# Optimization experiments

Hardware: AMD Instinct MI355X
Metric: run time of the kernel (lower is better)

Reference implementation:

```python
import jax, jax.numpy as jnp
import numpy as np

N, K = 1024, 128


def setup_inputs() -> dict:
    key = jax.random.key(0)
    k0, k1, k2, k3, k4 = jax.random.split(key, 5)
    beta = jax.random.uniform(k0, (N, N), dtype=jnp.float32)  # attention weights
    # omega must be invertible: small perturbation of identity, well-conditioned
    omega = jax.random.normal(k1, (N, K, K), dtype=jnp.float32) * 0.1 + jnp.eye(K, dtype=jnp.float32)
    # precisions are SPD in the physical model: A A^T / K + I
    A = jax.random.normal(k2, (N, K, K), dtype=jnp.float32)
    precision_p = jnp.einsum('nij,nkj->nik', A, A) / K + jnp.eye(K, dtype=jnp.float32)
    B = jax.random.normal(k3, (N, K, K), dtype=jnp.float32)
    precision_q = jnp.einsum('nij,nkj->nik', B, B) / K + jnp.eye(K, dtype=jnp.float32)
    C = jax.random.normal(k4, (K, K), dtype=jnp.float32)
    obs_precision = C @ C.T / K + jnp.eye(K, dtype=jnp.float32)
    return {
        'beta': beta,
        'omega': omega,
        'precision_p': precision_p,
        'precision_q': precision_q,
        'obs_precision': obs_precision,
    }


def reference(beta, omega, precision_p, precision_q, obs_precision):
    """Vectorized effective_mass_diagonal (Eq. 37).

    M_i = Lp_i + sum_{k!=i} beta_ik * Om_ik^{-T} Lq_k Om_ik^{-1}
               + (sum_{j!=i} beta_ji) * Lq_i + obs_precision
    with Om_ik = Om_i Om_k^{-1}, so Om_ik^{-1} = Om_k Om_i^{-1} and the
    sandwiched term factors as Om_i^{-T} (sum_k beta_ik * Om_k^T Lq_k Om_k) Om_i^{-1},
    turning the O(N^2) tiny-inverse loop into batched GEMMs + N inverses.
    """
    n = beta.shape[0]
    eye_mask = 1.0 - jnp.eye(n, dtype=beta.dtype)
    beta_nd = beta * eye_mask  # zero diagonal (k==i and j==i skipped)

    omega_inv = jnp.linalg.inv(omega)  # (N,K,K), batched
    # S_k = Omega_k^T Lq_k Omega_k, shape (N,K,K)
    S = jnp.einsum('nji,njk,nkl->nil', omega, precision_q, omega)
    # weighted accumulation over k != i: (N,N) x (N,K,K) -> (N,K,K)
    W = jnp.einsum('ik,kab->iab', beta_nd, S)
    # sandwich with Omega_i^{-T} ... Omega_i^{-1}
    cross = jnp.einsum('nji,njk,nkl->nil', omega_inv, W, omega_inv)

    col_sum = beta_nd.sum(axis=0)  # sum_j beta_ji, shape (N,)
    M = precision_p + cross + col_sum[:, None, None] * precision_q + obs_precision[None, :, :]
    return M  # (N, K, K)
```

## Files before the change

kernel.cpp:

```cpp
#include <hip/hip_runtime.h>

#define NN 1024
#define KK 128

typedef __attribute__((ext_vector_type(8))) short bf16x8;
typedef __attribute__((ext_vector_type(4))) float f32x4;
typedef __attribute__((ext_vector_type(8))) unsigned short u16x8;

__device__ __forceinline__ unsigned int bf16rne(float x) {
    unsigned int u = __float_as_uint(x);
    return (u + 0x7FFFu + ((u >> 16) & 1u)) >> 16;
}

__device__ __forceinline__ void split8(const float* xs, bf16x8& h8, bf16x8& l8) {
    #pragma unroll
    for (int j = 0; j < 8; ++j) {
        unsigned int hb = bf16rne(xs[j]);
        float hf = __uint_as_float(hb << 16);
        h8[j] = (short)hb;
        l8[j] = (short)bf16rne(xs[j] - hf);
    }
}

template<bool FINAL>
__global__ __launch_bounds__(512) void sandwich_mfma(
    const float* __restrict__ A_, const float* __restrict__ B_,
    float* __restrict__ Out,
    const float* __restrict__ Lp, const float* __restrict__ Lq,
    const float* __restrict__ obs, const float* __restrict__ beta)
{
    __shared__ short lds_buf[69632];
    short* Bth = lds_buf;
    short* Btl = lds_buf + 17408;
    short* Tth = lds_buf + 34816;
    short* Ttl = lds_buf + 52224;
    float* pan = (float*)(lds_buf + 34816);
    float* rowblk_  = (float*)(lds_buf + 34816);
    float* rowstar_ = rowblk_ + 1056;
    float* cpan_    = rowstar_ + 1056;
    __shared__ float wred[8];
    __shared__ float cs_sh;

    const int n    = blockIdx.x;
    const int tid  = threadIdx.x;
    const int lane = tid & 63;
    const int wid  = tid >> 6;
    const int wr   = wid >> 1;
    const int wc   = wid & 1;
    const int lm   = lane & 15;
    const int lk   = lane >> 4;
    const size_t base = (size_t)n * (KK * KK);

    if (FINAL) {
        float s = 0.f;
        for (int j = tid; j < NN; j += 512)
            if (j != n) s += beta[(size_t)j * NN + n];
        #pragma unroll
        for (int off = 32; off >= 1; off >>= 1) s += __shfl_down(s, off);
        if (lane == 0) wred[wid] = s;
        __syncthreads();
        if (tid == 0) {
            float t = 0.f;
            #pragma unroll
            for (int w = 0; w < 8; ++w) t += wred[w];
            cs_sh = t;
        }
    }

    if constexpr (!FINAL) {
        #pragma unroll
        for (int cp = 0; cp < 2; ++cp) {
            #pragma unroll
            for (int it = 0; it < 4; ++it) {
                int gid = it * 512 + tid;
                int k   = gid >> 4;
                int c4  = (gid & 15) * 4;
                *(float4*)&pan[k * 66 + c4] =
                    *(const float4*)(B_ + base + (size_t)k * KK + cp * 64 + c4);
            }
            __syncthreads();
            #pragma unroll
            for (int it = 0; it < 2; ++it) {
                int t  = it * 512 + tid;
                int c  = t >> 4;
                int ko = (t & 15) * 8;
                float xs[8];
                #pragma unroll
                for (int j = 0; j < 8; ++j) xs[j] = pan[(ko + j) * 66 + c];
                bf16x8 h8, l8;
                split8(xs, h8, l8);
                const int gc = cp * 64 + c;
                *(bf16x8*)&Bth[gc * 136 + ko] = h8;
                *(bf16x8*)&Btl[gc * 136 + ko] = l8;
            }
            __syncthreads();
        }
    } else {
        const int rg = tid >> 4;
        const int cg = tid & 15;
        const int r0 = rg * 4;
        const int c0 = cg * 8;

        float4 a4[4][2];
        #pragma unroll
        for (int i = 0; i < 4; ++i) {
            const float* src = B_ + base + (size_t)(r0 + i) * KK + c0;
            a4[i][0] = *(const float4*)(src);
            a4[i][1] = *(const float4*)(src + 4);
        }

        for (int g = 0; g < 32; ++g) {
            const int buf = g & 1;
            const int pgc = g >> 1;
            const int sub = g & 1;
            float* RB = rowblk_ + buf * 528;
            float* RS = rowstar_ + buf * 528;
            float* CP = cpan_ + buf * 512;

            if (rg == g) {
                #pragma unroll
                for (int p = 0; p < 4; ++p) {
                    *(float4*)&RB[p * 132 + c0]     = a4[p][0];
                    *(float4*)&RB[p * 132 + c0 + 4] = a4[p][1];
                }
            }
            if (cg == pgc) {
                if (sub == 0) {
                    #pragma unroll
                    for (int i = 0; i < 4; ++i)
                        *(float4*)&CP[(r0 + i) * 4] = a4[i][0];
                } else {
                    #pragma unroll
                    for (int i = 0; i < 4; ++i)
                        *(float4*)&CP[(r0 + i) * 4] = a4[i][1];
                }
            }
            __syncthreads();

            float4 p0 = *(const float4*)&RB[0 * 132 + 4 * g];
            float4 p1 = *(const float4*)&RB[1 * 132 + 4 * g];
            float4 p2 = *(const float4*)&RB[2 * 132 + 4 * g];
            float4 p3 = *(const float4*)&RB[3 * 132 + 4 * g];
            const float s0 = p0.x*p1.y - p1.x*p0.y;
            const float s1 = p0.x*p1.z - p1.x*p0.z;
            const float s2 = p0.x*p1.w - p1.x*p0.w;
            const float s3 = p0.y*p1.z - p1.y*p0.z;
            const float s4 = p0.y*p1.w - p1.y*p0.w;
            const float s5 = p0.z*p1.w - p1.z*p0.w;
            const float c5 = p2.z*p3.w - p3.z*p2.w;
            const float c4 = p2.y*p3.w - p3.y*p2.w;
            const float c3 = p2.y*p3.z - p3.y*p2.z;
            const float c2 = p2.x*p3.w - p3.x*p2.w;
            const float c1 = p2.x*p3.z - p3.x*p2.z;
            const float c0f = p2.x*p3.y - p3.x*p2.y;
            const float det = s0*c5 - s1*c4 + s2*c3 + s3*c2 - s4*c1 + s5*c0f;
            const float id  = 1.0f / det;

            {
                const int c = tid & 127;
                const float r0v = RB[0 * 132 + c];
                const float r1v = RB[1 * 132 + c];
                const float r2v = RB[2 * 132 + c];
                const float r3v = RB[3 * 132 + c];
                const int cl = c - 4 * g;
                const int pq = tid >> 7;
                if (pq == 0) {
                    const float Pi0 = ( p1.y*c5 - p1.z*c4 + p1.w*c3) * id;
                    const float Pi1 = (-p0.y*c5 + p0.z*c4 - p0.w*c3) * id;
                    const float Pi2 = ( p3.y*s5 - p3.z*s4 + p3.w*s3) * id;
                    const float Pi3 = (-p2.y*s5 + p2.z*s4 - p2.w*s3) * id;
                    float v = Pi0*r0v + Pi1*r1v + Pi2*r2v + Pi3*r3v;
                    if      (cl == 0) v += Pi0;
                    else if (cl == 1) v += Pi1;
                    else if (cl == 2) v += Pi2;
                    else if (cl == 3) v += Pi3;
                    RS[0 * 132 + c] = v;
                } else if (pq == 1) {
                    const float Pi0 = (-p1.x*c5 + p1.z*c2 - p1.w*c1) * id;
                    const float Pi1 = ( p0.x*c5 - p0.z*c2 + p0.w*c1) * id;
                    const float Pi2 = (-p3.x*s5 + p3.z*s2 - p3.w*s1) * id;
                    const float Pi3 = ( p2.x*s5 - p2.z*s2 + p2.w*s1) * id;
                    float v = Pi0*r0v + Pi1*r1v + Pi2*r2v + Pi3*r3v;
                    if      (cl == 0) v += Pi0;
                    else if (cl == 1) v += Pi1;
                    else if (cl == 2) v += Pi2;
                    else if (cl == 3) v += Pi3;
                    RS[1 * 132 + c] = v;
                } else if (pq == 2) {
                    const float Pi0 = ( p1.x*c4 - p1.y*c2 + p1.w*c0f) * id;
                    const float Pi1 = (-p0.x*c4 + p0.y*c2 - p0.w*c0f) * id;
                    const float Pi2 = ( p3.x*s4 - p3.y*s2 + p3.w*s0) * id;
                    const float Pi3 = (-p2.x*s4 + p2.y*s2 - p2.w*s0) * id;
                    float v = Pi0*r0v + Pi1*r1v + Pi2*r2v + Pi3*r3v;
                    if      (cl == 0) v += Pi0;
                    else if (cl == 1) v += Pi1;
                    else if (cl == 2) v += Pi2;
                    else if (cl == 3) v += Pi3;
                    RS[2 * 132 + c] = v;
                } else {
                    const float Pi0 = (-p1.x*c3 + p1.y*c1 - p1.z*c0f) * id;
                    const float Pi1 = ( p0.x*c3 - p0.y*c1 + p0.z*c0f) * id;
                    const float Pi2 = (-p3.x*s3 + p3.y*s1 - p3.z*s0) * id;
                    const float Pi3 = ( p2.x*s3 - p2.y*s1 + p2.z*s0) * id;
                    float v = Pi0*r0v + Pi1*r1v + Pi2*r2v + Pi3*r3v;
                    if      (cl == 0) v += Pi0;
                    else if (cl == 1) v += Pi1;
                    else if (cl == 2) v += Pi2;
                    else if (cl == 3) v += Pi3;
                    RS[3 * 132 + c] = v;
                }
            }
            __syncthreads();

            const bool piv_rg = (rg == g);
            #pragma unroll
            for (int h = 0; h < 2; ++h) {
                const int ch = c0 + h * 4;
                float4 rs0 = *(const float4*)&RS[0 * 132 + ch];
                float4 rs1 = *(const float4*)&RS[1 * 132 + ch];
                float4 rs2 = *(const float4*)&RS[2 * 132 + ch];
                float4 rs3 = *(const float4*)&RS[3 * 132 + ch];
                #pragma unroll
                for (int i = 0; i < 4; ++i) {
                    float4 f = *(const float4*)&CP[(r0 + i) * 4];
                    if (piv_rg) {
                        if (i == 0) f.x -= 1.0f;
                        else if (i == 1) f.y -= 1.0f;
                        else if (i == 2) f.z -= 1.0f;
                        else f.w -= 1.0f;
                    }
                    a4[i][h].x = fmaf(-f.x, rs0.x, fmaf(-f.y, rs1.x, fmaf(-f.z, rs2.x, fmaf(-f.w, rs3.x, a4[i][h].x))));
                    a4[i][h].y = fmaf(-f.x, rs0.y, fmaf(-f.y, rs1.y, fmaf(-f.z, rs2.y, fmaf(-f.w, rs3.y, a4[i][h].y))));
                    a4[i][h].z = fmaf(-f.x, rs0.z, fmaf(-f.y, rs1.z, fmaf(-f.z, rs2.z, fmaf(-f.w, rs3.z, a4[i][h].z))));
                    a4[i][h].w = fmaf(-f.x, rs0.w, fmaf(-f.y, rs1.w, fmaf(-f.z, rs2.w, fmaf(-f.w, rs3.w, a4[i][h].w))));
                }
            }
        }
        __syncthreads();

        #pragma unroll
        for (int i = 0; i < 4; ++i) {
            const int row = r0 + i;
            #pragma unroll
            for (int h = 0; h < 2; ++h) {
                float xs[4] = {a4[i][h].x, a4[i][h].y, a4[i][h].z, a4[i][h].w};
                #pragma unroll
                for (int j = 0; j < 4; ++j) {
                    const int col = c0 + h * 4 + j;
                    unsigned int hb = bf16rne(xs[j]);
                    Bth[col * 136 + row] = (short)hb;
                    Btl[col * 136 + row] =
                        (short)bf16rne(xs[j] - __uint_as_float(hb << 16));
                }
            }
        }
        __syncthreads();
    }

    f32x4 acc[2][4];
    #pragma unroll
    for (int a = 0; a < 2; ++a)
        #pragma unroll
        for (int b = 0; b < 4; ++b) acc[a][b] = (f32x4){0.f, 0.f, 0.f, 0.f};

    #pragma unroll 1
    for (int ks = 0; ks < 4; ++ks) {
        const int k0 = ks * 32;
        bf16x8 afh[2], afl[2], bfh[4], bfl[4];
        #pragma unroll
        for (int rt = 0; rt < 2; ++rt) {
            const int r = wr * 32 + rt * 16 + lm;
            const float* ap = A_ + base + (size_t)r * KK + k0 + lk * 8;
            float4 x0 = *(const float4*)ap;
            float4 x1 = *(const float4*)(ap + 4);
            float xs[8] = {x0.x, x0.y, x0.z, x0.w, x1.x, x1.y, x1.z, x1.w};
            split8(xs, afh[rt], afl[rt]);
        }
        #pragma unroll
        for (int ct = 0; ct < 4; ++ct) {
            const int c = wc * 64 + ct * 16 + lm;
            bfh[ct] = *(const bf16x8*)&Bth[c * 136 + k0 + lk * 8];
            bfl[ct] = *(const bf16x8*)&Btl[c * 136 + k0 + lk * 8];
        }
        #pragma unroll
        for (int rt = 0; rt < 2; ++rt)
            #pragma unroll
            for (int ct = 0; ct < 4; ++ct) {
                acc[rt][ct] = __builtin_amdgcn_mfma_f32_16x16x32_bf16(
                    afh[rt], bfh[ct], acc[rt][ct], 0, 0, 0);
                acc[rt][ct] = __builtin_amdgcn_mfma_f32_16x16x32_bf16(
                    afh[rt], bfl[ct], acc[rt][ct], 0, 0, 0);
                acc[rt][ct] = __builtin_amdgcn_mfma_f32_16x16x32_bf16(
                    afl[rt], bfh[ct], acc[rt][ct], 0, 0, 0);
            }
    }

    #pragma unroll
    for (int rt = 0; rt < 2; ++rt)
        #pragma unroll
        for (int ct = 0; ct < 4; ++ct) {
            const int col  = wc * 64 + ct * 16 + lm;
            const int row0 = wr * 32 + rt * 16 + lk * 4;
            unsigned short h[4], l[4];
            #pragma unroll
            for (int j = 0; j < 4; ++j) {
                float x = acc[rt][ct][j];
                unsigned int hb = bf16rne(x);
                h[j] = (unsigned short)hb;
                l[j] = (unsigned short)bf16rne(x - __uint_as_float(hb << 16));
            }
            *(ushort4*)&Tth[col * 136 + row0] = make_ushort4(h[0], h[1], h[2], h[3]);
            *(ushort4*)&Ttl[col * 136 + row0] = make_ushort4(l[0], l[1], l[2], l[3]);
        }
    __syncthreads();

    f32x4 acc2[2][4];
    #pragma unroll
    for (int a = 0; a < 2; ++a)
        #pragma unroll
        for (int b = 0; b < 4; ++b) acc2[a][b] = (f32x4){0.f, 0.f, 0.f, 0.f};

    #pragma unroll 1
    for (int ks = 0; ks < 4; ++ks) {
        const int k0 = ks * 32;
        bf16x8 afh[2], afl[2], bfh[4], bfl[4];
        #pragma unroll
        for (int rt = 0; rt < 2; ++rt) {
            const int r = wr * 32 + rt * 16 + lm;
            afh[rt] = *(const bf16x8*)&Bth[r * 136 + k0 + lk * 8];
            afl[rt] = *(const bf16x8*)&Btl[r * 136 + k0 + lk * 8];
        }
        #pragma unroll
        for (int ct = 0; ct < 4; ++ct) {
            const int c = wc * 64 + ct * 16 + lm;
            bfh[ct] = *(const bf16x8*)&Tth[c * 136 + k0 + lk * 8];
            bfl[ct] = *(const bf16x8*)&Ttl[c * 136 + k0 + lk * 8];
        }
        #pragma unroll
        for (int rt = 0; rt < 2; ++rt)
            #pragma unroll
            for (int ct = 0; ct < 4; ++ct) {
                acc2[rt][ct] = __builtin_amdgcn_mfma_f32_16x16x32_bf16(
                    afh[rt], bfh[ct], acc2[rt][ct], 0, 0, 0);
                acc2[rt][ct] = __builtin_amdgcn_mfma_f32_16x16x32_bf16(
                    afh[rt], bfl[ct], acc2[rt][ct], 0, 0, 0);
                acc2[rt][ct] = __builtin_amdgcn_mfma_f32_16x16x32_bf16(
                    afl[rt], bfh[ct], acc2[rt][ct], 0, 0, 0);
            }
    }

    const float csv = FINAL ? cs_sh : 0.f;
    #pragma unroll
    for (int rt = 0; rt < 2; ++rt)
        #pragma unroll
        for (int ct = 0; ct < 4; ++ct) {
            const int col  = wc * 64 + ct * 16 + lm;
            const int row0 = wr * 32 + rt * 16 + lk * 4;
            #pragma unroll
            for (int j = 0; j < 4; ++j) {
                const int row = row0 + j;
                float o = acc2[rt][ct][j];
                if (FINAL) {
                    o += Lp[base + (size_t)row * KK + col]
                       + csv * Lq[base + (size_t)row * KK + col]
                       + obs[(size_t)row * KK + col];
                }
                Out[base + (size_t)row * KK + col] = o;
            }
        }
}

__global__ __launch_bounds__(256) void split_transpose_kernel(
    const float* __restrict__ S,
    unsigned short* __restrict__ Th, unsigned short* __restrict__ Tl)
{
    __shared__ float tile[128][132];
    const int tid = threadIdx.x;
    const int c0  = blockIdx.x * 128;
    const int k0  = blockIdx.y * 128;

    #pragma unroll
    for (int it = 0; it < 16; ++it) {
        int gid = it * 256 + tid;
        int kk  = gid >> 5;
        int c4  = (gid & 31) * 4;
        float4 v = *(const float4*)(S + (size_t)(k0 + kk) * 16384 + c0 + c4);
        *(float4*)&tile[kk][c4] = v;
    }
    __syncthreads();
    #pragma unroll
    for (int it = 0; it < 8; ++it) {
        int gid = it * 256 + tid;
        int c   = gid >> 4;
        int kc  = (gid & 15) * 8;
        u16x8 h, l;
        #pragma unroll
        for (int j = 0; j < 8; ++j) {
            float x = tile[kc + j][c];
            unsigned int hb = bf16rne(x);
            float hf = __uint_as_float(hb << 16);
            h[j] = (unsigned short)hb;
            l[j] = (unsigned short)bf16rne(x - hf);
        }
        size_t o = (size_t)(c0 + c) * 1024 + k0 + kc;
        *(u16x8*)(Th + o) = h;
        *(u16x8*)(Tl + o) = l;
    }
}

__global__ __launch_bounds__(256) void beta_split_kernel(
    const float* __restrict__ beta,
    unsigned short* __restrict__ Bh, unsigned short* __restrict__ Bl)
{
    const int gid = blockIdx.x * 256 + threadIdx.x;
    const int r   = gid >> 8;
    const int c4  = (gid & 255) * 4;
    float4 v = *(const float4*)(beta + (size_t)r * NN + c4);
    if (r == c4 + 0) v.x = 0.f;
    if (r == c4 + 1) v.y = 0.f;
    if (r == c4 + 2) v.z = 0.f;
    if (r == c4 + 3) v.w = 0.f;
    float xs[4] = {v.x, v.y, v.z, v.w};
    unsigned short hs[4], ls[4];
    #pragma unroll
    for (int j = 0; j < 4; ++j) {
        unsigned int hb = bf16rne(xs[j]);
        hs[j] = (unsigned short)hb;
        ls[j] = (unsigned short)bf16rne(xs[j] - __uint_as_float(hb << 16));
    }
    *(ushort4*)(Bh + (size_t)r * NN + c4) = make_ushort4(hs[0], hs[1], hs[2], hs[3]);
    *(ushort4*)(Bl + (size_t)r * NN + c4) = make_ushort4(ls[0], ls[1], ls[2], ls[3]);
}

template<bool PRESPLIT>
__global__ __launch_bounds__(256) void gemm_beta_mfma(
    const float* __restrict__ beta,
    const unsigned short* __restrict__ Bth_g,
    const unsigned short* __restrict__ Btl_g,
    const unsigned short* __restrict__ Sth,
    const unsigned short* __restrict__ Stl,
    float* __restrict__ W)
{
    __shared__ unsigned short Ah[128][44], Al[128][44];
    __shared__ unsigned short Bh[128][44], Bl[128][44];

    const int tid  = threadIdx.x;
    const int lane = tid & 63;
    const int wid  = tid >> 6;
    const int wr   = wid >> 1, wc = wid & 1;
    const int lm   = lane & 15;
    const int lk   = lane >> 4;
    const int i0   = blockIdx.y * 128;
    const int cb   = blockIdx.x * 128;

    f32x4 acc[4][4];
    #pragma unroll
    for (int a = 0; a < 4; ++a)
        #pragma unroll
        for (int b = 0; b < 4; ++b) acc[a][b] = (f32x4){0.f, 0.f, 0.f, 0.f};

    for (int k0 = 0; k0 < 1024; k0 += 32) {
        if (PRESPLIT) {
            #pragma unroll
            for (int it = 0; it < 2; ++it) {
                int gid = it * 256 + tid;
                int r   = gid >> 2;
                int kc  = (gid & 3) * 8;
                size_t o = (size_t)(i0 + r) * NN + k0 + kc;
                *(u16x8*)&Ah[r][kc] = *(const u16x8*)(Bth_g + o);
                *(u16x8*)&Al[r][kc] = *(const u16x8*)(Btl_g + o);
            }
        } else {
            #pragma unroll
            for (int it = 0; it < 4; ++it) {
                int gid = it * 256 + tid;
                int r   = gid >> 3;
                int c4  = (gid & 7) * 4;
                int gi  = i0 + r;
                float4 v = *(const float4*)(beta + (size_t)gi * NN + k0 + c4);
                if (gi == k0 + c4 + 0) v.x = 0.f;
                if (gi == k0 + c4 + 1) v.y = 0.f;
                if (gi == k0 + c4 + 2) v.z = 0.f;
                if (gi == k0 + c4 + 3) v.w = 0.f;
                float xs[4] = {v.x, v.y, v.z, v.w};
                unsigned short hs[4], ls[4];
                #pragma unroll
                for (int j = 0; j < 4; ++j) {
                    unsigned int hb = bf16rne(xs[j]);
                    hs[j] = (unsigned short)hb;
                    ls[j] = (unsigned short)bf16rne(xs[j] - __uint_as_float(hb << 16));
                }
                *(ushort4*)&Ah[r][c4] = make_ushort4(hs[0], hs[1], hs[2], hs[3]);
                *(ushort4*)&Al[r][c4] = make_ushort4(ls[0], ls[1], ls[2], ls[3]);
            }
        }
        #pragma unroll
        for (int it = 0; it < 2; ++it) {
            int gid = it * 256 + tid;
            int c   = gid >> 2;
            int kc  = (gid & 3) * 8;
            size_t o = (size_t)(cb + c) * 1024 + k0 + kc;
            *(u16x8*)&Bh[c][kc] = *(const u16x8*)(Sth + o);
            *(u16x8*)&Bl[c][kc] = *(const u16x8*)(Stl + o);
        }
        __syncthreads();

        bf16x8 afh[4], afl[4], bfh[4], bfl[4];
        #pragma unroll
        for (int rt = 0; rt < 4; ++rt) {
            const int r = wr * 64 + rt * 16 + lm;
            afh[rt] = *(const bf16x8*)&Ah[r][lk * 8];
            afl[rt] = *(const bf16x8*)&Al[r][lk * 8];
        }
        #pragma unroll
        for (int ct = 0; ct < 4; ++ct) {
            const int c = wc * 64 + ct * 16 + lm;
            bfh[ct] = *(const bf16x8*)&Bh[c][lk * 8];
            bfl[ct] = *(const bf16x8*)&Bl[c][lk * 8];
        }
        #pragma unroll
        for (int rt = 0; rt < 4; ++rt)
            #pragma unroll
            for (int ct = 0; ct < 4; ++ct) {
                acc[rt][ct] = __builtin_amdgcn_mfma_f32_16x16x32_bf16(
                    afh[rt], bfh[ct], acc[rt][ct], 0, 0, 0);
                acc[rt][ct] = __builtin_amdgcn_mfma_f32_16x16x32_bf16(
                    afh[rt], bfl[ct], acc[rt][ct], 0, 0, 0);
                acc[rt][ct] = __builtin_amdgcn_mfma_f32_16x16x32_bf16(
                    afl[rt], bfh[ct], acc[rt][ct], 0, 0, 0);
            }
        __syncthreads();
    }

    #pragma unroll
    for (int rt = 0; rt < 4; ++rt)
        #pragma unroll
        for (int ct = 0; ct < 4; ++ct) {
            const int col = cb + wc * 64 + ct * 16 + lm;
            #pragma unroll
            for (int j = 0; j < 4; ++j) {
                const int row = i0 + wr * 64 + rt * 16 + lk * 4 + j;
                W[(size_t)row * 16384 + col] = acc[rt][ct][j];
            }
        }
}

extern "C" void kernel_launch(void* const* d_in, const int* in_sizes, int n_in,
                              void* d_out, int out_size, void* d_ws, size_t ws_size,
                              hipStream_t stream)
{
    const float* beta  = (const float*)d_in[0];
    const float* omega = (const float*)d_in[1];
    const float* Lp    = (const float*)d_in[2];
    const float* Lq    = (const float*)d_in[3];
    const float* obs   = (const float*)d_in[4];
    float* out = (float*)d_out;

    const size_t MATE = (size_t)NN * KK * KK;

    if (ws_size >= 2 * MATE * sizeof(float)) {
        float* S = (float*)d_ws;
        unsigned short* Sth = (unsigned short*)((char*)d_ws + MATE * sizeof(float));
        unsigned short* Stl = Sth + MATE;
        unsigned short* Bh  = (unsigned short*)d_ws;
        unsigned short* Bl  = Bh + (size_t)NN * NN;
        float* Wbuf = out;

        sandwich_mfma<false><<<dim3(NN), dim3(512), 0, stream>>>(
            Lq, omega, S, nullptr, nullptr, nullptr, nullptr);
        split_transpose_kernel<<<dim3(128, 8), dim3(256), 0, stream>>>(S, Sth, Stl);
        beta_split_kernel<<<dim3(1024), dim3(256), 0, stream>>>(beta, Bh, Bl);
        gemm_beta_mfma<true><<<dim3(128, 8), dim3(256), 0, stream>>>(
            beta, Bh, Bl, Sth, Stl, Wbuf);
        sandwich_mfma<true><<<dim3(NN), dim3(512), 0, stream>>>(
            Wbuf, omega, out, Lp, Lq, obs, beta);
    } else {
        float* S = (float*)d_ws;
        unsigned short* Sth = (unsigned short*)out;
        unsigned short* Stl = Sth + MATE;
        float* Wbuf = (float*)d_ws;

        sandwich_mfma<false><<<dim3(NN), dim3(512), 0, stream>>>(
            Lq, omega, S, nullptr, nullptr, nullptr, nullptr);
        split_transpose_kernel<<<dim3(128, 8), dim3(256), 0, stream>>>(S, Sth, Stl);
        gemm_beta_mfma<false><<<dim3(128, 8), dim3(256), 0, stream>>>(
            beta, nullptr, nullptr, Sth, Stl, Wbuf);
        sandwich_mfma<true><<<dim3(NN), dim3(512), 0, stream>>>(
            Wbuf, omega, out, Lp, Lq, obs, beta);
    }
}
```

Before: 451.2 us.

## Move omega inversion out of final sandwich and co-schedule it with beta GEMM

```diff
diff --git a/kernel.cpp b/kernel.cpp
--- a/kernel.cpp
+++ b/kernel.cpp
@@ -35,9 +35,6 @@
     short* Tth = lds_buf + 34816;
     short* Ttl = lds_buf + 52224;
     float* pan = (float*)(lds_buf + 34816);
-    float* rowblk_  = (float*)(lds_buf + 34816);
-    float* rowstar_ = rowblk_ + 1056;
-    float* cpan_    = rowstar_ + 1056;
     __shared__ float wred[8];
     __shared__ float cs_sh;
 
@@ -67,192 +64,30 @@
         }
     }
 
-    if constexpr (!FINAL) {
-        #pragma unroll
-        for (int cp = 0; cp < 2; ++cp) {
-            #pragma unroll
-            for (int it = 0; it < 4; ++it) {
-                int gid = it * 512 + tid;
-                int k   = gid >> 4;
-                int c4  = (gid & 15) * 4;
-                *(float4*)&pan[k * 66 + c4] =
-                    *(const float4*)(B_ + base + (size_t)k * KK + cp * 64 + c4);
-            }
-            __syncthreads();
-            #pragma unroll
-            for (int it = 0; it < 2; ++it) {
-                int t  = it * 512 + tid;
-                int c  = t >> 4;
-                int ko = (t & 15) * 8;
-                float xs[8];
-                #pragma unroll
-                for (int j = 0; j < 8; ++j) xs[j] = pan[(ko + j) * 66 + c];
-                bf16x8 h8, l8;
-                split8(xs, h8, l8);
-                const int gc = cp * 64 + c;
-                *(bf16x8*)&Bth[gc * 136 + ko] = h8;
-                *(bf16x8*)&Btl[gc * 136 + ko] = l8;
-            }
-            __syncthreads();
-        }
-    } else {
-        const int rg = tid >> 4;
-        const int cg = tid & 15;
-        const int r0 = rg * 4;
-        const int c0 = cg * 8;
-
-        float4 a4[4][2];
-        #pragma unroll
-        for (int i = 0; i < 4; ++i) {
-            const float* src = B_ + base + (size_t)(r0 + i) * KK + c0;
-            a4[i][0] = *(const float4*)(src);
-            a4[i][1] = *(const float4*)(src + 4);
-        }
-
-        for (int g = 0; g < 32; ++g) {
-            const int buf = g & 1;
-            const int pgc = g >> 1;
-            const int sub = g & 1;
-            float* RB = rowblk_ + buf * 528;
-            float* RS = rowstar_ + buf * 528;
-            float* CP = cpan_ + buf * 512;
-
-            if (rg == g) {
-                #pragma unroll
-                for (int p = 0; p < 4; ++p) {
-                    *(float4*)&RB[p * 132 + c0]     = a4[p][0];
-                    *(float4*)&RB[p * 132 + c0 + 4] = a4[p][1];
-                }
-            }
-            if (cg == pgc) {
-                if (sub == 0) {
-                    #pragma unroll
-                    for (int i = 0; i < 4; ++i)
-                        *(float4*)&CP[(r0 + i) * 4] = a4[i][0];
-                } else {
-                    #pragma unroll
-                    for (int i = 0; i < 4; ++i)
-                        *(float4*)&CP[(r0 + i) * 4] = a4[i][1];
-                }
-            }
-            __syncthreads();
-
-            float4 p0 = *(const float4*)&RB[0 * 132 + 4 * g];
-            float4 p1 = *(const float4*)&RB[1 * 132 + 4 * g];
-            float4 p2 = *(const float4*)&RB[2 * 132 + 4 * g];
-            float4 p3 = *(const float4*)&RB[3 * 132 + 4 * g];
-            const float s0 = p0.x*p1.y - p1.x*p0.y;
-            const float s1 = p0.x*p1.z - p1.x*p0.z;
-            const float s2 = p0.x*p1.w - p1.x*p0.w;
-            const float s3 = p0.y*p1.z - p1.y*p0.z;
-            const float s4 = p0.y*p1.w - p1.y*p0.w;
-            const float s5 = p0.z*p1.w - p1.z*p0.w;
-            const float c5 = p2.z*p3.w - p3.z*p2.w;
-            const float c4 = p2.y*p3.w - p3.y*p2.w;
-            const float c3 = p2.y*p3.z - p3.y*p2.z;
-            const float c2 = p2.x*p3.w - p3.x*p2.w;
-            const float c1 = p2.x*p3.z - p3.x*p2.z;
-            const float c0f = p2.x*p3.y - p3.x*p2.y;
-            const float det = s0*c5 - s1*c4 + s2*c3 + s3*c2 - s4*c1 + s5*c0f;
-            const float id  = 1.0f / det;
-
-            {
-                const int c = tid & 127;
-                const float r0v = RB[0 * 132 + c];
-                const float r1v = RB[1 * 132 + c];
-                const float r2v = RB[2 * 132 + c];
-                const float r3v = RB[3 * 132 + c];
-                const int cl = c - 4 * g;
-                const int pq = tid >> 7;
-                if (pq == 0) {
-                    const float Pi0 = ( p1.y*c5 - p1.z*c4 + p1.w*c3) * id;
-                    const float Pi1 = (-p0.y*c5 + p0.z*c4 - p0.w*c3) * id;
-                    const float Pi2 = ( p3.y*s5 - p3.z*s4 + p3.w*s3) * id;
-                    const float Pi3 = (-p2.y*s5 + p2.z*s4 - p2.w*s3) * id;
-                    float v = Pi0*r0v + Pi1*r1v + Pi2*r2v + Pi3*r3v;
-                    if      (cl == 0) v += Pi0;
-                    else if (cl == 1) v += Pi1;
-                    else if (cl == 2) v += Pi2;
-                    else if (cl == 3) v += Pi3;
-                    RS[0 * 132 + c] = v;
-                } else if (pq == 1) {
-                    const float Pi0 = (-p1.x*c5 + p1.z*c2 - p1.w*c1) * id;
-                    const float Pi1 = ( p0.x*c5 - p0.z*c2 + p0.w*c1) * id;
-                    const float Pi2 = (-p3.x*s5 + p3.z*s2 - p3.w*s1) * id;
-                    const float Pi3 = ( p2.x*s5 - p2.z*s2 + p2.w*s1) * id;
-                    float v = Pi0*r0v + Pi1*r1v + Pi2*r2v + Pi3*r3v;
-                    if      (cl == 0) v += Pi0;
-                    else if (cl == 1) v += Pi1;
-                    else if (cl == 2) v += Pi2;
-                    else if (cl == 3) v += Pi3;
-                    RS[1 * 132 + c] = v;
-                } else if (pq == 2) {
-                    const float Pi0 = ( p1.x*c4 - p1.y*c2 + p1.w*c0f) * id;
-                    const float Pi1 = (-p0.x*c4 + p0.y*c2 - p0.w*c0f) * id;
-                    const float Pi2 = ( p3.x*s4 - p3.y*s2 + p3.w*s0) * id;
-                    const float Pi3 = (-p2.x*s4 + p2.y*s2 - p2.w*s0) * id;
-                    float v = Pi0*r0v + Pi1*r1v + Pi2*r2v + Pi3*r3v;
-                    if      (cl == 0) v += Pi0;
-                    else if (cl == 1) v += Pi1;
-                    else if (cl == 2) v += Pi2;
-                    else if (cl == 3) v += Pi3;
-                    RS[2 * 132 + c] = v;
-                } else {
-                    const float Pi0 = (-p1.x*c3 + p1.y*c1 - p1.z*c0f) * id;
-                    const float Pi1 = ( p0.x*c3 - p0.y*c1 + p0.z*c0f) * id;
-                    const float Pi2 = (-p3.x*s3 + p3.y*s1 - p3.z*s0) * id;
-                    const float Pi3 = ( p2.x*s3 - p2.y*s1 + p2.z*s0) * id;
-                    float v = Pi0*r0v + Pi1*r1v + Pi2*r2v + Pi3*r3v;
-                    if      (cl == 0) v += Pi0;
-                    else if (cl == 1) v += Pi1;
-                    else if (cl == 2) v += Pi2;
-                    else if (cl == 3) v += Pi3;
-                    RS[3 * 132 + c] = v;
-                }
-            }
-            __syncthreads();
-
-            const bool piv_rg = (rg == g);
-            #pragma unroll
-            for (int h = 0; h < 2; ++h) {
-                const int ch = c0 + h * 4;
-                float4 rs0 = *(const float4*)&RS[0 * 132 + ch];
-                float4 rs1 = *(const float4*)&RS[1 * 132 + ch];
-                float4 rs2 = *(const float4*)&RS[2 * 132 + ch];
-                float4 rs3 = *(const float4*)&RS[3 * 132 + ch];
-                #pragma unroll
-                for (int i = 0; i < 4; ++i) {
-                    float4 f = *(const float4*)&CP[(r0 + i) * 4];
-                    if (piv_rg) {
-                        if (i == 0) f.x -= 1.0f;
-                        else if (i == 1) f.y -= 1.0f;
-                        else if (i == 2) f.z -= 1.0f;
-                        else f.w -= 1.0f;
-                    }
-                    a4[i][h].x = fmaf(-f.x, rs0.x, fmaf(-f.y, rs1.x, fmaf(-f.z, rs2.x, fmaf(-f.w, rs3.x, a4[i][h].x))));
-                    a4[i][h].y = fmaf(-f.x, rs0.y, fmaf(-f.y, rs1.y, fmaf(-f.z, rs2.y, fmaf(-f.w, rs3.y, a4[i][h].y))));
-                    a4[i][h].z = fmaf(-f.x, rs0.z, fmaf(-f.y, rs1.z, fmaf(-f.z, rs2.z, fmaf(-f.w, rs3.z, a4[i][h].z))));
-                    a4[i][h].w = fmaf(-f.x, rs0.w, fmaf(-f.y, rs1.w, fmaf(-f.z, rs2.w, fmaf(-f.w, rs3.w, a4[i][h].w))));
-                }
-            }
-        }
-        __syncthreads();
-
-        #pragma unroll
-        for (int i = 0; i < 4; ++i) {
-            const int row = r0 + i;
-            #pragma unroll
-            for (int h = 0; h < 2; ++h) {
-                float xs[4] = {a4[i][h].x, a4[i][h].y, a4[i][h].z, a4[i][h].w};
-                #pragma unroll
-                for (int j = 0; j < 4; ++j) {
-                    const int col = c0 + h * 4 + j;
-                    unsigned int hb = bf16rne(xs[j]);
-                    Bth[col * 136 + row] = (short)hb;
-                    Btl[col * 136 + row] =
-                        (short)bf16rne(xs[j] - __uint_as_float(hb << 16));
-                }
-            }
+    #pragma unroll
+    for (int cp = 0; cp < 2; ++cp) {
+        #pragma unroll
+        for (int it = 0; it < 4; ++it) {
+            int gid = it * 512 + tid;
+            int k   = gid >> 4;
+            int c4  = (gid & 15) * 4;
+            *(float4*)&pan[k * 66 + c4] =
+                *(const float4*)(B_ + base + (size_t)k * KK + cp * 64 + c4);
+        }
+        __syncthreads();
+        #pragma unroll
+        for (int it = 0; it < 2; ++it) {
+            int t  = it * 512 + tid;
+            int c  = t >> 4;
+            int ko = (t & 15) * 8;
+            float xs[8];
+            #pragma unroll
+            for (int j = 0; j < 8; ++j) xs[j] = pan[(ko + j) * 66 + c];
+            bf16x8 h8, l8;
+            split8(xs, h8, l8);
+            const int gc = cp * 64 + c;
+            *(bf16x8*)&Bth[gc * 136 + ko] = h8;
+            *(bf16x8*)&Btl[gc * 136 + ko] = l8;
         }
         __syncthreads();
     }
@@ -408,118 +243,73 @@
     }
 }
 
-__global__ __launch_bounds__(256) void beta_split_kernel(
+__device__ __forceinline__ void gemm_body(
     const float* __restrict__ beta,
-    unsigned short* __restrict__ Bh, unsigned short* __restrict__ Bl)
-{
-    const int gid = blockIdx.x * 256 + threadIdx.x;
-    const int r   = gid >> 8;
-    const int c4  = (gid & 255) * 4;
-    float4 v = *(const float4*)(beta + (size_t)r * NN + c4);
-    if (r == c4 + 0) v.x = 0.f;
-    if (r == c4 + 1) v.y = 0.f;
-    if (r == c4 + 2) v.z = 0.f;
-    if (r == c4 + 3) v.w = 0.f;
-    float xs[4] = {v.x, v.y, v.z, v.w};
-    unsigned short hs[4], ls[4];
-    #pragma unroll
-    for (int j = 0; j < 4; ++j) {
-        unsigned int hb = bf16rne(xs[j]);
-        hs[j] = (unsigned short)hb;
-        ls[j] = (unsigned short)bf16rne(xs[j] - __uint_as_float(hb << 16));
-    }
-    *(ushort4*)(Bh + (size_t)r * NN + c4) = make_ushort4(hs[0], hs[1], hs[2], hs[3]);
-    *(ushort4*)(Bl + (size_t)r * NN + c4) = make_ushort4(ls[0], ls[1], ls[2], ls[3]);
-}
-
-template<bool PRESPLIT>
-__global__ __launch_bounds__(256) void gemm_beta_mfma(
-    const float* __restrict__ beta,
-    const unsigned short* __restrict__ Bth_g,
-    const unsigned short* __restrict__ Btl_g,
     const unsigned short* __restrict__ Sth,
     const unsigned short* __restrict__ Stl,
-    float* __restrict__ W)
-{
-    __shared__ unsigned short Ah[128][44], Al[128][44];
-    __shared__ unsigned short Bh[128][44], Bl[128][44];
-
-    const int tid  = threadIdx.x;
+    float* __restrict__ W,
+    int cb_blk, int ib_blk, int tid, char* smem)
+{
+    unsigned short* Ah = (unsigned short*)smem;
+    unsigned short* Al = Ah + 128 * 44;
+    unsigned short* Bh = Al + 128 * 44;
+    unsigned short* Bl = Bh + 128 * 44;
+
     const int lane = tid & 63;
     const int wid  = tid >> 6;
-    const int wr   = wid >> 1, wc = wid & 1;
+    const int wr   = wid >> 1;
+    const int wc   = wid & 1;
     const int lm   = lane & 15;
     const int lk   = lane >> 4;
-    const int i0   = blockIdx.y * 128;
-    const int cb   = blockIdx.x * 128;
-
-    f32x4 acc[4][4];
-    #pragma unroll
-    for (int a = 0; a < 4; ++a)
+    const int i0   = ib_blk * 128;
+    const int cbase = cb_blk * 128;
+
+    f32x4 acc[2][4];
+    #pragma unroll
+    for (int a = 0; a < 2; ++a)
         #pragma unroll
         for (int b = 0; b < 4; ++b) acc[a][b] = (f32x4){0.f, 0.f, 0.f, 0.f};
 
+    const int ar = tid >> 2;
+    const int akc = (tid & 3) * 8;
+
     for (int k0 = 0; k0 < 1024; k0 += 32) {
-        if (PRESPLIT) {
-            #pragma unroll
-            for (int it = 0; it < 2; ++it) {
-                int gid = it * 256 + tid;
-                int r   = gid >> 2;
-                int kc  = (gid & 3) * 8;
-                size_t o = (size_t)(i0 + r) * NN + k0 + kc;
-                *(u16x8*)&Ah[r][kc] = *(const u16x8*)(Bth_g + o);
-                *(u16x8*)&Al[r][kc] = *(const u16x8*)(Btl_g + o);
-            }
-        } else {
-            #pragma unroll
-            for (int it = 0; it < 4; ++it) {
-                int gid = it * 256 + tid;
-                int r   = gid >> 3;
-                int c4  = (gid & 7) * 4;
-                int gi  = i0 + r;
-                float4 v = *(const float4*)(beta + (size_t)gi * NN + k0 + c4);
-                if (gi == k0 + c4 + 0) v.x = 0.f;
-                if (gi == k0 + c4 + 1) v.y = 0.f;
-                if (gi == k0 + c4 + 2) v.z = 0.f;
-                if (gi == k0 + c4 + 3) v.w = 0.f;
-                float xs[4] = {v.x, v.y, v.z, v.w};
-                unsigned short hs[4], ls[4];
-                #pragma unroll
-                for (int j = 0; j < 4; ++j) {
-                    unsigned int hb = bf16rne(xs[j]);
-                    hs[j] = (unsigned short)hb;
-                    ls[j] = (unsigned short)bf16rne(xs[j] - __uint_as_float(hb << 16));
-                }
-                *(ushort4*)&Ah[r][c4] = make_ushort4(hs[0], hs[1], hs[2], hs[3]);
-                *(ushort4*)&Al[r][c4] = make_ushort4(ls[0], ls[1], ls[2], ls[3]);
-            }
-        }
-        #pragma unroll
-        for (int it = 0; it < 2; ++it) {
-            int gid = it * 256 + tid;
-            int c   = gid >> 2;
-            int kc  = (gid & 3) * 8;
-            size_t o = (size_t)(cb + c) * 1024 + k0 + kc;
-            *(u16x8*)&Bh[c][kc] = *(const u16x8*)(Sth + o);
-            *(u16x8*)&Bl[c][kc] = *(const u16x8*)(Stl + o);
-        }
-        __syncthreads();
-
-        bf16x8 afh[4], afl[4], bfh[4], bfl[4];
-        #pragma unroll
-        for (int rt = 0; rt < 4; ++rt) {
-            const int r = wr * 64 + rt * 16 + lm;
-            afh[rt] = *(const bf16x8*)&Ah[r][lk * 8];
-            afl[rt] = *(const bf16x8*)&Al[r][lk * 8];
+        {
+            const int gi = i0 + ar;
+            const float* bp = beta + (size_t)gi * NN + k0 + akc;
+            float4 v0 = *(const float4*)bp;
+            float4 v1 = *(const float4*)(bp + 4);
+            float xs[8] = {v0.x, v0.y, v0.z, v0.w, v1.x, v1.y, v1.z, v1.w};
+            #pragma unroll
+            for (int e = 0; e < 8; ++e)
+                if (gi == k0 + akc + e) xs[e] = 0.f;
+            bf16x8 h8, l8;
+            split8(xs, h8, l8);
+            *(bf16x8*)&Ah[ar * 44 + akc] = h8;
+            *(bf16x8*)&Al[ar * 44 + akc] = l8;
+        }
+        {
+            size_t o = (size_t)(cbase + ar) * 1024 + k0 + akc;
+            *(u16x8*)&Bh[ar * 44 + akc] = *(const u16x8*)(Sth + o);
+            *(u16x8*)&Bl[ar * 44 + akc] = *(const u16x8*)(Stl + o);
+        }
+        __syncthreads();
+
+        bf16x8 afh[2], afl[2], bfh[4], bfl[4];
+        #pragma unroll
+        for (int rt = 0; rt < 2; ++rt) {
+            const int r = wr * 32 + rt * 16 + lm;
+            afh[rt] = *(const bf16x8*)&Ah[r * 44 + lk * 8];
+            afl[rt] = *(const bf16x8*)&Al[r * 44 + lk * 8];
         }
         #pragma unroll
         for (int ct = 0; ct < 4; ++ct) {
             const int c = wc * 64 + ct * 16 + lm;
-            bfh[ct] = *(const bf16x8*)&Bh[c][lk * 8];
-            bfl[ct] = *(const bf16x8*)&Bl[c][lk * 8];
-        }
-        #pragma unroll
-        for (int rt = 0; rt < 4; ++rt)
+            bfh[ct] = *(const bf16x8*)&Bh[c * 44 + lk * 8];
+            bfl[ct] = *(const bf16x8*)&Bl[c * 44 + lk * 8];
+        }
+        #pragma unroll
+        for (int rt = 0; rt < 2; ++rt)
             #pragma unroll
             for (int ct = 0; ct < 4; ++ct) {
                 acc[rt][ct] = __builtin_amdgcn_mfma_f32_16x16x32_bf16(
@@ -533,16 +323,210 @@
     }
 
     #pragma unroll
-    for (int rt = 0; rt < 4; ++rt)
+    for (int rt = 0; rt < 2; ++rt)
         #pragma unroll
         for (int ct = 0; ct < 4; ++ct) {
-            const int col = cb + wc * 64 + ct * 16 + lm;
+            const int col = cbase + wc * 64 + ct * 16 + lm;
             #pragma unroll
             for (int j = 0; j < 4; ++j) {
-                const int row = i0 + wr * 64 + rt * 16 + lk * 4 + j;
+                const int row = i0 + wr * 32 + rt * 16 + lk * 4 + j;
                 W[(size_t)row * 16384 + col] = acc[rt][ct][j];
             }
         }
+}
+
+__device__ __forceinline__ void invert_body(
+    const float* __restrict__ Om, float* __restrict__ Inv,
+    int n, int tid, char* smem)
+{
+    float* rowblk  = (float*)smem;
+    float* rowstar = rowblk + 1056;
+    float* cpan    = rowstar + 1056;
+
+    const int rg  = tid >> 4;
+    const int cg  = tid & 15;
+    const int r0  = rg * 4;
+    const int c0  = cg * 8;
+    const size_t base = (size_t)n * (KK * KK);
+
+    float4 a4[4][2];
+    #pragma unroll
+    for (int i = 0; i < 4; ++i) {
+        const float* src = Om + base + (size_t)(r0 + i) * KK + c0;
+        a4[i][0] = *(const float4*)(src);
+        a4[i][1] = *(const float4*)(src + 4);
+    }
+
+    for (int g = 0; g < 32; ++g) {
+        const int buf = g & 1;
+        const int pgc = g >> 1;
+        const int sub = g & 1;
+        float* RB = rowblk + buf * 528;
+        float* RS = rowstar + buf * 528;
+        float* CP = cpan + buf * 512;
+
+        if (rg == g) {
+            #pragma unroll
+            for (int p = 0; p < 4; ++p) {
+                *(float4*)&RB[p * 132 + c0]     = a4[p][0];
+                *(float4*)&RB[p * 132 + c0 + 4] = a4[p][1];
+            }
+        }
+        if (cg == pgc) {
+            if (sub == 0) {
+                #pragma unroll
+                for (int i = 0; i < 4; ++i)
+                    *(float4*)&CP[(r0 + i) * 4] = a4[i][0];
+            } else {
+                #pragma unroll
+                for (int i = 0; i < 4; ++i)
+                    *(float4*)&CP[(r0 + i) * 4] = a4[i][1];
+            }
+        }
+        __syncthreads();
+
+        float4 p0 = *(const float4*)&RB[0 * 132 + 4 * g];
+        float4 p1 = *(const float4*)&RB[1 * 132 + 4 * g];
+        float4 p2 = *(const float4*)&RB[2 * 132 + 4 * g];
+        float4 p3 = *(const float4*)&RB[3 * 132 + 4 * g];
+        const float s0 = p0.x*p1.y - p1.x*p0.y;
+        const float s1 = p0.x*p1.z - p1.x*p0.z;
+        const float s2 = p0.x*p1.w - p1.x*p0.w;
+        const float s3 = p0.y*p1.z - p1.y*p0.z;
+        const float s4 = p0.y*p1.w - p1.y*p0.w;
+        const float s5 = p0.z*p1.w - p1.z*p0.w;
+        const float c5 = p2.z*p3.w - p3.z*p2.w;
+        const float c4 = p2.y*p3.w - p3.y*p2.w;
+        const float c3 = p2.y*p3.z - p3.y*p2.z;
+        const float c2 = p2.x*p3.w - p3.x*p2.w;
+        const float c1 = p2.x*p3.z - p3.x*p2.z;
+        const float c0f = p2.x*p3.y - p3.x*p2.y;
+        const float det = s0*c5 - s1*c4 + s2*c3 + s3*c2 - s4*c1 + s5*c0f;
+        const float id  = 1.0f / det;
+
+        {
+            const int c = tid & 127;
+            const float r0v = RB[0 * 132 + c];
+            const float r1v = RB[1 * 132 + c];
+            const float r2v = RB[2 * 132 + c];
+            const float r3v = RB[3 * 132 + c];
+            const int cl = c - 4 * g;
+            const int pq = tid >> 7;
+            if (pq == 0) {
+                const float Pi0 = ( p1.y*c5 - p1.z*c4 + p1.w*c3) * id;
+                const float Pi1 = (-p0.y*c5 + p0.z*c4 - p0.w*c3) * id;
+                const float Pi2 = ( p3.y*s5 - p3.z*s4 + p3.w*s3) * id;
+                const float Pi3 = (-p2.y*s5 + p2.z*s4 - p2.w*s3) * id;
+                float v = Pi0*r0v + Pi1*r1v + Pi2*r2v + Pi3*r3v;
+                if      (cl == 0) v += Pi0;
+                else if (cl == 1) v += Pi1;
+                else if (cl == 2) v += Pi2;
+                else if (cl == 3) v += Pi3;
+                RS[0 * 132 + c] = v;
+            } else if (pq == 1) {
+                const float Pi0 = (-p1.x*c5 + p1.z*c2 - p1.w*c1) * id;
+                const float Pi1 = ( p0.x*c5 - p0.z*c2 + p0.w*c1) * id;
+                const float Pi2 = (-p3.x*s5 + p3.z*s2 - p3.w*s1) * id;
+                const float Pi3 = ( p2.x*s5 - p2.z*s2 + p2.w*s1) * id;
+                float v = Pi0*r0v + Pi1*r1v + Pi2*r2v + Pi3*r3v;
+                if      (cl == 0) v += Pi0;
+                else if (cl == 1) v += Pi1;
+                else if (cl == 2) v += Pi2;
+                else if (cl == 3) v += Pi3;
+                RS[1 * 132 + c] = v;
+            } else if (pq == 2) {
+                const float Pi0 = ( p1.x*c4 - p1.y*c2 + p1.w*c0f) * id;
+                const float Pi1 = (-p0.x*c4 + p0.y*c2 - p0.w*c0f) * id;
+                const float Pi2 = ( p3.x*s4 - p3.y*s2 + p3.w*s0) * id;
+                const float Pi3 = (-p2.x*s4 + p2.y*s2 - p2.w*s0) * id;
+                float v = Pi0*r0v + Pi1*r1v + Pi2*r2v + Pi3*r3v;
+                if      (cl == 0) v += Pi0;
+                else if (cl == 1) v += Pi1;
+                else if (cl == 2) v += Pi2;
+                else if (cl == 3) v += Pi3;
+                RS[2 * 132 + c] = v;
+            } else {
+                const float Pi0 = (-p1.x*c3 + p1.y*c1 - p1.z*c0f) * id;
+                const float Pi1 = ( p0.x*c3 - p0.y*c1 + p0.z*c0f) * id;
+                const float Pi2 = (-p3.x*s3 + p3.y*s1 - p3.z*s0) * id;
+                const float Pi3 = ( p2.x*s3 - p2.y*s1 + p2.z*s0) * id;
+                float v = Pi0*r0v + Pi1*r1v + Pi2*r2v + Pi3*r3v;
+                if      (cl == 0) v += Pi0;
+                else if (cl == 1) v += Pi1;
+                else if (cl == 2) v += Pi2;
+                else if (cl == 3) v += Pi3;
+                RS[3 * 132 + c] = v;
+            }
+        }
+        __syncthreads();
+
+        const bool piv_rg = (rg == g);
+        #pragma unroll
+        for (int h = 0; h < 2; ++h) {
+            const int ch = c0 + h * 4;
+            float4 rs0 = *(const float4*)&RS[0 * 132 + ch];
+            float4 rs1 = *(const float4*)&RS[1 * 132 + ch];
+            float4 rs2 = *(const float4*)&RS[2 * 132 + ch];
+            float4 rs3 = *(const float4*)&RS[3 * 132 + ch];
+            #pragma unroll
+            for (int i = 0; i < 4; ++i) {
+                float4 f = *(const float4*)&CP[(r0 + i) * 4];
+                if (piv_rg) {
+                    if (i == 0) f.x -= 1.0f;
+                    else if (i == 1) f.y -= 1.0f;
+                    else if (i == 2) f.z -= 1.0f;
+                    else f.w -= 1.0f;
+                }
+                a4[i][h].x = fmaf(-f.x, rs0.x, fmaf(-f.y, rs1.x, fmaf(-f.z, rs2.x, fmaf(-f.w, rs3.x, a4[i][h].x))));
+                a4[i][h].y = fmaf(-f.x, rs0.y, fmaf(-f.y, rs1.y, fmaf(-f.z, rs2.y, fmaf(-f.w, rs3.y, a4[i][h].y))));
+                a4[i][h].z = fmaf(-f.x, rs0.z, fmaf(-f.y, rs1.z, fmaf(-f.z, rs2.z, fmaf(-f.w, rs3.z, a4[i][h].z))));
+                a4[i][h].w = fmaf(-f.x, rs0.w, fmaf(-f.y, rs1.w, fmaf(-f.z, rs2.w, fmaf(-f.w, rs3.w, a4[i][h].w))));
+            }
+        }
+    }
+
+    #pragma unroll
+    for (int i = 0; i < 4; ++i) {
+        float* dst = Inv + base + (size_t)(r0 + i) * KK + c0;
+        *(float4*)(dst)     = a4[i][0];
+        *(float4*)(dst + 4) = a4[i][1];
+    }
+}
+
+__global__ __launch_bounds__(512) void gemm_invert_fused(
+    const float* __restrict__ beta,
+    const unsigned short* __restrict__ Sth,
+    const unsigned short* __restrict__ Stl,
+    float* __restrict__ W,
+    const float* __restrict__ Om,
+    float* __restrict__ Inv)
+{
+    __shared__ __align__(16) char smem[45056];
+    const int b = blockIdx.x;
+    if ((b & 1) == 0) {
+        const int g = b >> 1;
+        gemm_body(beta, Sth, Stl, W, g & 127, g >> 7, threadIdx.x, smem);
+    } else {
+        const int n = b >> 1;
+        invert_body(Om, Inv, n, threadIdx.x, smem);
+    }
+}
+
+__global__ __launch_bounds__(512) void gemm_kernel(
+    const float* __restrict__ beta,
+    const unsigned short* __restrict__ Sth,
+    const unsigned short* __restrict__ Stl,
+    float* __restrict__ W)
+{
+    __shared__ __align__(16) char smem[45056];
+    gemm_body(beta, Sth, Stl, W, blockIdx.x, blockIdx.y, threadIdx.x, smem);
+}
+
+__global__ __launch_bounds__(512) void invert_kernel(
+    const float* __restrict__ Om, float* __restrict__ Inv)
+{
+    __shared__ __align__(16) char smem[12544];
+    invert_body(Om, Inv, blockIdx.x, threadIdx.x, smem);
 }
 
 extern "C" void kernel_launch(void* const* d_in, const int* in_sizes, int n_in,
@@ -562,30 +546,29 @@
         float* S = (float*)d_ws;
         unsigned short* Sth = (unsigned short*)((char*)d_ws + MATE * sizeof(float));
         unsigned short* Stl = Sth + MATE;
-        unsigned short* Bh  = (unsigned short*)d_ws;
-        unsigned short* Bl  = Bh + (size_t)NN * NN;
+        float* Inv  = (float*)d_ws;
         float* Wbuf = out;
 
         sandwich_mfma<false><<<dim3(NN), dim3(512), 0, stream>>>(
             Lq, omega, S, nullptr, nullptr, nullptr, nullptr);
         split_transpose_kernel<<<dim3(128, 8), dim3(256), 0, stream>>>(S, Sth, Stl);
-        beta_split_kernel<<<dim3(1024), dim3(256), 0, stream>>>(beta, Bh, Bl);
-        gemm_beta_mfma<true><<<dim3(128, 8), dim3(256), 0, stream>>>(
-            beta, Bh, Bl, Sth, Stl, Wbuf);
+        gemm_invert_fused<<<dim3(2048), dim3(512), 0, stream>>>(
+            beta, Sth, Stl, Wbuf, omega, Inv);
         sandwich_mfma<true><<<dim3(NN), dim3(512), 0, stream>>>(
-            Wbuf, omega, out, Lp, Lq, obs, beta);
+            Wbuf, Inv, out, Lp, Lq, obs, beta);
     } else {
         float* S = (float*)d_ws;
         unsigned short* Sth = (unsigned short*)out;
         unsigned short* Stl = Sth + MATE;
         float* Wbuf = (float*)d_ws;
+        float* Inv  = out;
 
         sandwich_mfma<false><<<dim3(NN), dim3(512), 0, stream>>>(
             Lq, omega, S, nullptr, nullptr, nullptr, nullptr);
         split_transpose_kernel<<<dim3(128, 8), dim3(256), 0, stream>>>(S, Sth, Stl);
-        gemm_beta_mfma<false><<<dim3(128, 8), dim3(256), 0, stream>>>(
-            beta, nullptr, nullptr, Sth, Stl, Wbuf);
+        gemm_kernel<<<dim3(128, 8), dim3(512), 0, stream>>>(beta, Sth, Stl, Wbuf);
+        invert_kernel<<<dim3(NN), dim3(512), 0, stream>>>(omega, Inv);
         sandwich_mfma<true><<<dim3(NN), dim3(512), 0, stream>>>(
-            Wbuf, omega, out, Lp, Lq, obs, beta);
-    }
-}
+            Wbuf, Inv, out, Lp, Lq, obs, beta);
+    }
+}
```

Result: slower. 1.083 ms (+140.0%).
